# Kernel optimization log

Hardware: AMD Instinct MI355X
Metric: run time of the kernel (lower is better)

The kernel has to match this reference:

```python
import jax, jax.numpy as jnp
import numpy as np

B, S, HID = 2, 2048, 2048
H, KV, D = 16, 4, 128
G = H // KV  # kv groups
THETA = 10000.0


def setup_inputs() -> dict:
    key = jax.random.key(0)
    ks = jax.random.split(key, 6)
    x = jax.random.normal(ks[0], (B, S, HID), dtype=jnp.float32)
    wq = jax.random.normal(ks[1], (HID, H * D), dtype=jnp.float32) * 0.02
    wk = jax.random.normal(ks[2], (HID, KV * D), dtype=jnp.float32) * 0.02
    wv = jax.random.normal(ks[3], (HID, KV * D), dtype=jnp.float32) * 0.02
    wo = jax.random.normal(ks[4], (H * D, HID), dtype=jnp.float32) * 0.02
    # RoPE freqs: complex exp(i * pos * theta^{-2j/D}) -> cos/sin of shape [S, D//2]
    inv_freq = 1.0 / (THETA ** (jnp.arange(0, D, 2, dtype=jnp.float32) / D))
    ang = jnp.arange(S, dtype=jnp.float32)[:, None] * inv_freq[None, :]
    return {"x": x, "freqs_cos": jnp.cos(ang), "freqs_sin": jnp.sin(ang),
            "wq": wq, "wk": wk, "wv": wv, "wo": wo}


def _apply_rope(t, cos, sin):
    # t: [B, h, S, D]; cos/sin: [S, D//2]; complex multiply on interleaved pairs
    tr = t.reshape(*t.shape[:-1], -1, 2)
    x1, x2 = tr[..., 0], tr[..., 1]
    c = cos[None, None, :, :]
    s = sin[None, None, :, :]
    out = jnp.stack([x1 * c - x2 * s, x1 * s + x2 * c], axis=-1)
    return out.reshape(t.shape)


def reference(x, freqs_cos, freqs_sin, wq, wk, wv, wo):
    b, s, _ = x.shape
    q = (x @ wq).reshape(b, s, H, D).transpose(0, 2, 1, 3)   # [B,H,S,D]
    k = (x @ wk).reshape(b, s, KV, D).transpose(0, 2, 1, 3)  # [B,KV,S,D]
    v = (x @ wv).reshape(b, s, KV, D).transpose(0, 2, 1, 3)
    q = _apply_rope(q, freqs_cos, freqs_sin)
    k = _apply_rope(k, freqs_cos, freqs_sin)
    # GQA: group Q heads per KV head instead of expanding K/V
    qg = q.reshape(b, KV, G, s, D)
    scale = 1.0 / jnp.sqrt(jnp.asarray(D, dtype=x.dtype))
    scores = jnp.einsum('bkgqd,bksd->bkgqs', qg, k) * scale  # [B,KV,G,S,S]
    causal = jnp.tril(jnp.ones((s, s), dtype=bool))
    scores = jnp.where(causal[None, None, None], scores, jnp.finfo(scores.dtype).min)
    attn = jax.nn.softmax(scores, axis=-1)
    out = jnp.einsum('bkgqs,bksd->bkgqd', attn, v)           # [B,KV,G,S,D]
    out = out.reshape(b, H, s, D).transpose(0, 2, 1, 3).reshape(b, s, H * D)
    return (out @ wo, k, v)
```

## Files before the change

### kernel.cpp

```cpp
#include <hip/hip_runtime.h>
#include <stdint.h>

#define BB 2
#define SS 2048
#define HIDD 2048
#define HH 16
#define KVH 4
#define DD 128
#define KDIM 2048

typedef short bf16x4 __attribute__((ext_vector_type(4)));
typedef short bf16x8 __attribute__((ext_vector_type(8)));
typedef float f32x4 __attribute__((ext_vector_type(4)));
typedef float f32x16 __attribute__((ext_vector_type(16)));

__device__ __forceinline__ unsigned short f2b(float f) {
  union { float f; unsigned u; } v; v.f = f;
  unsigned r = v.u + 0x7FFFu + ((v.u >> 16) & 1u);
  return (unsigned short)(r >> 16);
}

__device__ __forceinline__ float b2f(unsigned short u) {
  union { unsigned u; float f; } v; v.u = ((unsigned)u) << 16;
  return v.f;
}

__device__ __forceinline__ unsigned cvtpk_bf16(float a, float b) {
  unsigned r;
  asm("v_cvt_pk_bf16_f32 %0, %1, %2" : "=v"(r) : "v"(a), "v"(b));
  return r;
}

__device__ __forceinline__ void gload16(const unsigned short* g, unsigned short* l) {
  __builtin_amdgcn_global_load_lds(
      (const __attribute__((address_space(1))) unsigned int*)(g),
      (__attribute__((address_space(3))) unsigned int*)(l), 16, 0, 0);
}

__device__ __forceinline__ bf16x8 ldT(const char* lds, int byteoff) {
  union { bf16x8 v; int4 q; } u;
  u.q = *reinterpret_cast<const int4*>(lds + byteoff);
  return u.v;
}

template <int N>
__device__ __forceinline__ void waitv() {
  if constexpr (N == 0) asm volatile("s_waitcnt vmcnt(0)" ::: "memory");
  else if constexpr (N == 1) asm volatile("s_waitcnt vmcnt(1)" ::: "memory");
  else if constexpr (N == 2) asm volatile("s_waitcnt vmcnt(2)" ::: "memory");
  else if constexpr (N == 3) asm volatile("s_waitcnt vmcnt(3)" ::: "memory");
  else if constexpr (N == 4) asm volatile("s_waitcnt vmcnt(4)" ::: "memory");
  else if constexpr (N == 5) asm volatile("s_waitcnt vmcnt(5)" ::: "memory");
  else asm volatile("s_waitcnt vmcnt(6)" ::: "memory");
}


__global__ __launch_bounds__(256) void k_convert(const float* __restrict__ in,
                                                 unsigned short* __restrict__ out, int n4) {
  int i = blockIdx.x * 256 + threadIdx.x;
  int stride = gridDim.x * 256;
  for (; i < n4; i += stride) {
    float4 v = reinterpret_cast<const float4*>(in)[i];
    ushort4 o;
    o.x = f2b(v.x); o.y = f2b(v.y); o.z = f2b(v.z); o.w = f2b(v.w);
    int ci = i & 511;
    int t = ci & 7;
    int ci2 = (ci & ~7) | ((t & 3) << 1) | (t >> 2);
    reinterpret_cast<ushort4*>(out)[(i & ~511) | ci2] = o;
  }
}

__global__ __launch_bounds__(256) void k_transpose(const float* __restrict__ in,
                                                   unsigned short* __restrict__ out,
                                                   int K, int N) {
  __shared__ float tile[32][33];
  int n0 = blockIdx.x * 32, k0 = blockIdx.y * 32;
  int tx = threadIdx.x, ty = threadIdx.y;
#pragma unroll
  for (int j = 0; j < 32; j += 8)
    tile[ty + j][tx] = in[(size_t)(k0 + ty + j) * N + n0 + tx];
  __syncthreads();
  int kp = ((tx >> 2) & 3) * 8 + (tx & 3) + ((tx >> 4) << 2);
#pragma unroll
  for (int j = 0; j < 32; j += 8)
    out[(size_t)(n0 + ty + j) * K + k0 + kp] = f2b(tile[tx][ty + j]);
}

__global__ __launch_bounds__(512, 4) void k_gemm12(
    const unsigned short* __restrict__ A, const unsigned short* __restrict__ Bt,
    unsigned short* __restrict__ qws, unsigned short* __restrict__ kws,
    unsigned short* __restrict__ vTws, float* __restrict__ koutF,
    float* __restrict__ voutF, const float* __restrict__ cosT,
    const float* __restrict__ sinT) {
  __shared__ __align__(16) unsigned short lA[2][128 * 64];
  __shared__ __align__(16) unsigned short lB[2][192 * 64];
  const int bid = blockIdx.y * gridDim.x + blockIdx.x;
  const int swz = (bid & 7) * 64 + (bid >> 3);
  const int rowbase = (swz & 31) * 128;
  const int colbase = (swz >> 5) * 192;
  const int tid = threadIdx.x;
  const int wv = tid >> 6, lane = tid & 63;
  const int wr = wv >> 2, wc = wv & 3;
  const int g = lane >> 4, c = lane & 15;

  const unsigned short* aSrc[2];
  const unsigned short* bSrc[3];
  int aDst[2], bDst[3];
#pragma unroll
  for (int j = 0; j < 2; ++j) {
    int idx = j * 512 + tid;
    int row = idx >> 3, sl = idx & 7;
    int gch = sl ^ (row & 7);
    aSrc[j] = A + (size_t)(rowbase + row) * KDIM + gch * 8;
    aDst[j] = idx * 8;
  }
#pragma unroll
  for (int j = 0; j < 3; ++j) {
    int idx = j * 512 + tid;
    int row = idx >> 3, sl = idx & 7;
    int gch = sl ^ (row & 7);
    bSrc[j] = Bt + (size_t)(colbase + row) * KDIM + gch * 8;
    bDst[j] = idx * 8;
  }

  f32x4 acc[4][3] = {};
  const int NT = KDIM / 64;

  auto STAGE = [&](int buf, int kt) {
#pragma unroll
    for (int j = 0; j < 2; ++j)
      gload16(aSrc[j] + kt * 64, &lA[buf][0] + aDst[j]);
#pragma unroll
    for (int j = 0; j < 3; ++j)
      gload16(bSrc[j] + kt * 64, &lB[buf][0] + bDst[j]);
  };

  STAGE(0, 0);
  STAGE(1, 1);

  for (int t = 0; t < NT; ++t) {
    if (t + 1 < NT) { waitv<5>(); } else { waitv<0>(); }
    __builtin_amdgcn_sched_barrier(0);
    __builtin_amdgcn_s_barrier();

    const unsigned short* la = lA[t & 1];
    const unsigned short* lb = lB[t & 1];
    bf16x8 bfr[3][2];
#pragma unroll
    for (int nn = 0; nn < 3; ++nn) {
      int sr = wc * 48 + nn * 16 + c;
#pragma unroll
      for (int kk = 0; kk < 2; ++kk) {
        int slot = (kk * 4 + g) ^ (sr & 7);
        bfr[nn][kk] = *reinterpret_cast<const bf16x8*>(lb + sr * 64 + slot * 8);
      }
    }
#pragma unroll
    for (int mm = 0; mm < 4; ++mm) {
      int sr = wr * 64 + mm * 16 + c;
      int slot0 = g ^ (sr & 7);
      int slot1 = (4 + g) ^ (sr & 7);
      bf16x8 af0 = *reinterpret_cast<const bf16x8*>(la + sr * 64 + slot0 * 8);
      bf16x8 af1 = *reinterpret_cast<const bf16x8*>(la + sr * 64 + slot1 * 8);
#pragma unroll
      for (int nn = 0; nn < 3; ++nn) {
        acc[mm][nn] = __builtin_amdgcn_mfma_f32_16x16x32_bf16(af0, bfr[nn][0], acc[mm][nn], 0, 0, 0);
        acc[mm][nn] = __builtin_amdgcn_mfma_f32_16x16x32_bf16(af1, bfr[nn][1], acc[mm][nn], 0, 0, 0);
      }
    }
    asm volatile("s_waitcnt lgkmcnt(0)" ::: "memory");
    __builtin_amdgcn_s_barrier();
    if (t + 2 < NT) STAGE(t & 1, t + 2);
  }

#pragma unroll
  for (int m = 0; m < 4; ++m) {
#pragma unroll
    for (int n = 0; n < 3; ++n) {
#pragma unroll
      for (int i = 0; i < 4; ++i) {
        float val = acc[m][n][i];
        float partner = __shfl_xor(val, 1, 64);
        int R = rowbase + wr * 64 + m * 16 + g * 4 + i;
        int Cc = colbase + wc * 48 + n * 16 + c;
        int b = R >> 11, s = R & 2047;
        int d = Cc & 127;
        int j = d >> 1;
        float cs = cosT[s * 64 + j], sn = sinT[s * 64 + j];
        float ro = ((d & 1) == 0) ? (val * cs - partner * sn)
                                  : (partner * sn + val * cs);
        if (Cc < 2048) {
          int h = Cc >> 7;
          qws[((size_t)(b * HH + h) * SS + s) * DD + d] = f2b(ro);
        } else if (Cc < 2560) {
          int kvh = (Cc - 2048) >> 7;
          size_t idx = ((size_t)(b * KVH + kvh) * SS + s) * DD + d;
          koutF[idx] = ro;
          int d16 = d & 15;
          int dp = (d & ~15) | (d16 & 3) | ((d16 & 4) << 1) | ((d16 & 8) >> 1);
          kws[((size_t)(b * KVH + kvh) * SS + s) * DD + dp] = f2b(ro);
        } else {
          int kvh = (Cc - 2560) >> 7;
          size_t idx = ((size_t)(b * KVH + kvh) * SS + s) * DD + d;
          voutF[idx] = val;
          int s16 = s & 15;
          int sp = (s & ~15) | (s16 & 3) | ((s16 & 4) << 1) | ((s16 & 8) >> 1);
          vTws[((size_t)(b * KVH + kvh) * DD + d) * SS + sp] = f2b(val);
        }
      }
    }
  }
}

template <int EPI, int BM>
__global__ __launch_bounds__(512) void k_gemm8(
    const unsigned short* __restrict__ A, const unsigned short* __restrict__ Bt,
    float* __restrict__ outF,
    const float* __restrict__ cosT, const float* __restrict__ sinT) {
  constexpr int LA = BM / 128;
  constexpr int LB = 2;
  constexpr int ASTR = BM * 64;
  constexpr int BSTR = 256 * 64;
  constexpr int MF = BM / 64;
  constexpr int LSH = (BM == 256) ? 6 : 5;
  extern __shared__ __align__(16) unsigned short smem[];
  unsigned short* lAb = smem;
  unsigned short* lBb = smem + 2 * ASTR;

  const int bid = blockIdx.y * gridDim.x + blockIdx.x;
  const int nwg = gridDim.x * gridDim.y;
  const int mt = gridDim.x;
  const int swz = (bid & 7) * (nwg >> 3) + (bid >> 3);
  const int rowbase = (swz % mt) * BM;
  const int colbase = (swz / mt) * 256;

  const int tid = threadIdx.x;
  const int wv = tid >> 6, lane = tid & 63;
  const int wr = wv >> 2, wc = wv & 3;
  const int g = lane >> 4, c = lane & 15;

  const int srow8 = lane >> 3;
  const int gch = (lane & 7) ^ srow8;
  const unsigned short* aS[LA][2];
  const unsigned short* bS[2][2];
  int aOff[LA][2], bOff[2][2];
#pragma unroll
  for (int j = 0; j < LA; ++j)
#pragma unroll
    for (int h = 0; h < 2; ++h) {
      int s = wv * LA + j;
      int q = s * 8 + srow8;
      int rA = (q >> LSH) * (BM / 2) + h * (BM / 4) + (q & (BM / 4 - 1));
      aS[j][h] = A + (size_t)(rowbase + rA) * KDIM + gch * 8;
      aOff[j][h] = (h * (BM / 2) + s * 8) * 64;
    }
#pragma unroll
  for (int j = 0; j < 2; ++j)
#pragma unroll
    for (int h = 0; h < 2; ++h) {
      int s = wv * 2 + j;
      int q = s * 8 + srow8;
      int rB = (q >> 5) * 64 + h * 32 + (q & 31);
      bS[j][h] = Bt + (size_t)(colbase + rB) * KDIM + gch * 8;
      bOff[j][h] = (h * 128 + s * 8) * 64;
    }

  f32x4 acc[2 * MF][4] = {};
  bf16x8 af[MF][2], bfr[4][2];
  const int NT = KDIM / 64;

#define STAGE_A(buf, kt, h)                                               \
  _Pragma("unroll") for (int j = 0; j < LA; ++j)                          \
      gload16(aS[j][h] + (kt) * 64, lAb + (buf) * ASTR + aOff[j][h]);
#define STAGE_B(buf, kt, h)                                               \
  _Pragma("unroll") for (int j = 0; j < 2; ++j)                           \
      gload16(bS[j][h] + (kt) * 64, lBb + (buf) * BSTR + bOff[j][h]);
#define LDA(buf, mh)                                                      \
  _Pragma("unroll") for (int mm = 0; mm < MF; ++mm) {                     \
    int sr = (mh) * (BM / 2) + wr * (BM / 4) + mm * 16 + c;               \
    _Pragma("unroll") for (int kk = 0; kk < 2; ++kk) {                    \
      int slot = (kk * 4 + g) ^ (c & 7);                                  \
      af[mm][kk] = *reinterpret_cast<const bf16x8*>(                      \
          lAb + (buf) * ASTR + sr * 64 + slot * 8);                       \
    } }
#define LDB(buf, nh)                                                      \
  _Pragma("unroll") for (int nn = 0; nn < 2; ++nn) {                      \
    int sr = (nh) * 128 + wc * 32 + nn * 16 + c;                          \
    _Pragma("unroll") for (int kk = 0; kk < 2; ++kk) {                    \
      int slot = (kk * 4 + g) ^ (c & 7);                                  \
      bfr[(nh) * 2 + nn][kk] = *reinterpret_cast<const bf16x8*>(          \
          lBb + (buf) * BSTR + sr * 64 + slot * 8);                       \
    } }
#define MM(mh, nh)                                                        \
  _Pragma("unroll") for (int mm = 0; mm < MF; ++mm)                       \
  _Pragma("unroll") for (int nn = 0; nn < 2; ++nn)                        \
  _Pragma("unroll") for (int kk = 0; kk < 2; ++kk)                        \
    acc[(mh) * MF + mm][(nh) * 2 + nn] =                                  \
        __builtin_amdgcn_mfma_f32_16x16x32_bf16(                          \
            af[mm][kk], bfr[(nh) * 2 + nn][kk],                           \
            acc[(mh) * MF + mm][(nh) * 2 + nn], 0, 0, 0);
#define SCHB __builtin_amdgcn_sched_barrier(0);
#define SB __builtin_amdgcn_s_barrier();
#define LGKM asm volatile("s_waitcnt lgkmcnt(0)" ::: "memory");
#define MFMAWIN(mh, nh)                                                   \
  LGKM SCHB __builtin_amdgcn_s_setprio(1);                                \
  MM(mh, nh) __builtin_amdgcn_s_setprio(0); SCHB SB

  STAGE_A(0, 0, 0) STAGE_B(0, 0, 0) STAGE_B(0, 0, 1) STAGE_A(0, 0, 1)
  waitv<LA + LB>(); SCHB SB

  for (int kt = 0; kt < NT - 1; ++kt) {
    const int buf = kt & 1, nbuf = buf ^ 1;
    LDA(buf, 0) LDB(buf, 0)
    STAGE_A(nbuf, kt + 1, 0)
    waitv<2 * LA>(); SCHB SB
    MFMAWIN(0, 0)
    LDB(buf, 1)
    STAGE_B(nbuf, kt + 1, 0)
    waitv<LA + LB>(); SCHB SB
    MFMAWIN(0, 1)
    LDA(buf, 1)
    STAGE_B(nbuf, kt + 1, 1)
    SCHB SB
    MFMAWIN(1, 0)
    STAGE_A(nbuf, kt + 1, 1)
    waitv<LA + LB>(); SCHB SB
    MFMAWIN(1, 1)
  }
  {
    const int buf = (NT - 1) & 1;
    LDA(buf, 0) LDB(buf, 0)
    waitv<LA>(); SCHB SB
    MFMAWIN(0, 0)
    LDB(buf, 1)
    waitv<0>(); SCHB SB
    MFMAWIN(0, 1)
    LDA(buf, 1)
    SCHB SB
    MFMAWIN(1, 0)
    __builtin_amdgcn_s_setprio(1);
    MM(1, 1)
    __builtin_amdgcn_s_setprio(0);
  }

#pragma unroll
  for (int m = 0; m < 2 * MF; ++m)
#pragma unroll
    for (int n = 0; n < 4; ++n)
#pragma unroll
      for (int i = 0; i < 4; ++i) {
        int R = rowbase + wr * (BM / 2) + m * 16 + g * 4 + i;
        int Cc = colbase + wc * 64 + n * 16 + c;
        outF[(size_t)R * 2048 + Cc] = acc[m][n][i];
      }
  (void)cosT; (void)sinT;
#undef STAGE_A
#undef STAGE_B
#undef LDA
#undef LDB
#undef MM
#undef SCHB
#undef SB
#undef LGKM
#undef MFMAWIN
}

__constant__ int JC[24] = {7,15,15,14,14,6,13,13,12,12,5,11,11,10,10,4,9,9,8,8,3,2,1,0};
__constant__ int JP[24] = {0,0,1, 0,1, 0,0,1, 0,1, 0,0,1, 0,1, 0,0,1, 0,1, 0,0,0,0};

__global__ __launch_bounds__(256, 2) void k_attn(const unsigned short* __restrict__ qws,
                                                 const unsigned short* __restrict__ kws,
                                                 const unsigned short* __restrict__ vT,
                                                 unsigned short* __restrict__ aows,
                                                 unsigned short* __restrict__ pO,
                                                 float* __restrict__ pml) {
  __shared__ __align__(16) char lds[2][32768];
  const int tid = threadIdx.x;
  const int lane = tid & 63;
  const int w = tid >> 6;
  const int lq = lane & 31;
  const int hi = lane >> 5;

  const int bid = blockIdx.x;
  const int j = bid >> 5;
  const int y = bid & 31;
  const int head = 4 * (y & 7) + ((y >> 3) & 3);
  const int c = JC[j];
  const int part = JP[j];
  const bool split = (c >= 8);
  const int tstart = split ? (part ? (c + 1) : 0) : 0;
  const int tend = split ? (part ? (2 * c + 2) : (c + 1)) : (2 * c + 2);

  const int b = head >> 4, h = head & 15;
  const int kv = h >> 2;
  const int q0w = c * 128 + w * 32;
  const int qg = q0w + lq;
  const float cl2 = 0.12751743f;

  const unsigned short* qp = qws + ((size_t)(b * HH + h) * SS + qg) * DD;
  bf16x8 qf[8];
#pragma unroll
  for (int ks = 0; ks < 8; ++ks) {
    union { bf16x8 v8; bf16x4 v4[2]; } u;
    const unsigned short* p = qp + ks * 16 + hi * 4;
    u.v4[0] = *reinterpret_cast<const bf16x4*>(p);
    u.v4[1] = *reinterpret_cast<const bf16x4*>(p + 8);
    qf[ks] = u.v8;
  }

  const unsigned short* kbase = kws + (size_t)(b * KVH + kv) * SS * DD;
  const unsigned short* vbase = vT + (size_t)(b * KVH + kv) * DD * SS;

  const unsigned short* kSrc[4];
  const unsigned short* vSrc[4];
  int ldsOff[4];
#pragma unroll
  for (int j2 = 0; j2 < 4; ++j2) {
    int i = w + 4 * j2;
    int ks = i >> 1, half = i & 1;
    kSrc[j2] = kbase + (size_t)(half * 32 + (lane >> 1)) * DD + ks * 16 + (lane & 1) * 8;
    int kkv = i >> 2, d0v = i & 3;
    vSrc[j2] = vbase + (size_t)(d0v * 32 + (lane >> 1)) * SS + kkv * 16 + (lane & 1) * 8;
    ldsOff[j2] = i * 1024;
  }

  auto STAGE = [&](int t, int buf) {
    char* lK = lds[buf];
    char* lV = lds[buf] + 16384;
#pragma unroll
    for (int j2 = 0; j2 < 4; ++j2) {
      gload16(kSrc[j2] + (size_t)t * 64 * DD, (unsigned short*)(lK + ldsOff[j2]));
      gload16(vSrc[j2] + (size_t)t * 64, (unsigned short*)(lV + ldsOff[j2]));
    }
  };

  f32x16 o[4] = {};
  float mrow = -1e30f, lrow = 0.f;

  STAGE(tstart, 0);
  STAGE(tstart + 1, 1);
  asm volatile("s_waitcnt vmcnt(8)" ::: "memory");
  __builtin_amdgcn_sched_barrier(0);
  __builtin_amdgcn_s_barrier();

  for (int t = tstart; t < tend; ++t) {
    const int cur = (t - tstart) & 1;

    if (t * 64 <= q0w + 31) {
      const char* lK = lds[cur];
      const char* lV = lds[cur] + 16384;
      const bool full2 = (t * 64 + 32 <= q0w + 31);

      f32x16 s0 = {}, s1 = {};
      __builtin_amdgcn_s_setprio(1);
#pragma unroll
      for (int ks = 0; ks < 8; ++ks) {
        int off = ks * 2048 + lq * 32 + hi * 16;
        s0 = __builtin_amdgcn_mfma_f32_32x32x16_bf16(ldT(lK, off), qf[ks], s0, 0, 0, 0);
      }
      if (full2) {
#pragma unroll
        for (int ks = 0; ks < 8; ++ks) {
          int off = ks * 2048 + 1024 + lq * 32 + hi * 16;
          s1 = __builtin_amdgcn_mfma_f32_32x32x16_bf16(ldT(lK, off), qf[ks], s1, 0, 0, 0);
        }
      }
      __builtin_amdgcn_s_setprio(0);

      const int kq = t * 64 + 4 * hi - qg;
      float p[32];
      float rowmax = -1e30f;
      const bool m0 = (t * 64 + 31) > q0w;
#pragma unroll
      for (int r = 0; r < 16; ++r) {
        float v = s0[r] * cl2;
        if (m0) {
          int kl = (r & 3) + 8 * (r >> 2);
          if (kq + kl > 0) v = -1e30f;
        }
        p[r] = v;
        rowmax = fmaxf(rowmax, v);
      }
      if (full2) {
        const bool m1 = (t * 64 + 63) > q0w;
#pragma unroll
        for (int r = 0; r < 16; ++r) {
          float v = s1[r] * cl2;
          if (m1) {
            int kl = 32 + (r & 3) + 8 * (r >> 2);
            if (kq + kl > 0) v = -1e30f;
          }
          p[16 + r] = v;
          rowmax = fmaxf(rowmax, v);
        }
      }
      rowmax = fmaxf(rowmax, __shfl_xor(rowmax, 32, 64));

      if (__any(rowmax > mrow + 8.f)) {
        float mnew = fmaxf(mrow, rowmax);
        float fac = exp2f(mrow - mnew);
        mrow = mnew;
        lrow *= fac;
#pragma unroll
        for (int d0 = 0; d0 < 4; ++d0)
#pragma unroll
          for (int r = 0; r < 16; ++r) o[d0][r] *= fac;
      }

      float rsum = 0.f;
#pragma unroll
      for (int e = 0; e < 16; ++e) { p[e] = exp2f(p[e] - mrow); rsum += p[e]; }
      if (full2) {
#pragma unroll
        for (int e = 16; e < 32; ++e) { p[e] = exp2f(p[e] - mrow); rsum += p[e]; }
      }
      rsum += __shfl_xor(rsum, 32, 64);
      lrow += rsum;

      bf16x8 pf[4];
#pragma unroll
      for (int s4 = 0; s4 < 2; ++s4) {
        union { bf16x8 v; unsigned u[4]; } pu;
        int base = s4 * 8;
#pragma unroll
        for (int jj = 0; jj < 4; ++jj)
          pu.u[jj] = cvtpk_bf16(p[base + 2 * jj], p[base + 2 * jj + 1]);
        pf[s4] = pu.v;
      }
      if (full2) {
#pragma unroll
        for (int s4 = 2; s4 < 4; ++s4) {
          union { bf16x8 v; unsigned u[4]; } pu;
          int base = 16 + (s4 - 2) * 8;
#pragma unroll
          for (int jj = 0; jj < 4; ++jj)
            pu.u[jj] = cvtpk_bf16(p[base + 2 * jj], p[base + 2 * jj + 1]);
          pf[s4] = pu.v;
        }
      }

      __builtin_amdgcn_s_setprio(1);
#pragma unroll
      for (int d0 = 0; d0 < 4; ++d0)
#pragma unroll
        for (int kk = 0; kk < 2; ++kk) {
          int off = (kk * 4 + d0) * 1024 + lq * 32 + hi * 16;
          o[d0] = __builtin_amdgcn_mfma_f32_32x32x16_bf16(ldT(lV, off), pf[kk], o[d0], 0, 0, 0);
        }
      if (full2) {
#pragma unroll
        for (int d0 = 0; d0 < 4; ++d0)
#pragma unroll
          for (int kk = 2; kk < 4; ++kk) {
            int off = (kk * 4 + d0) * 1024 + lq * 32 + hi * 16;
            o[d0] = __builtin_amdgcn_mfma_f32_32x32x16_bf16(ldT(lV, off), pf[kk], o[d0], 0, 0, 0);
          }
      }
      __builtin_amdgcn_s_setprio(0);
    }

    if (t + 1 < tend) {
      __builtin_amdgcn_s_barrier();
      if (t + 2 < tend) {
        STAGE(t + 2, cur);
        asm volatile("s_waitcnt vmcnt(8)" ::: "memory");
      } else {
        asm volatile("s_waitcnt vmcnt(0)" ::: "memory");
      }
      __builtin_amdgcn_sched_barrier(0);
      __builtin_amdgcn_s_barrier();
    }
  }

  if (!split) {
    float linv = 1.f / lrow;
    unsigned short* op = aows + ((size_t)(b * SS + qg)) * 2048 + h * 128;
#pragma unroll
    for (int d0 = 0; d0 < 4; ++d0)
#pragma unroll
      for (int rq = 0; rq < 4; ++rq) {
        unsigned w0 = cvtpk_bf16(o[d0][rq * 4 + 0] * linv, o[d0][rq * 4 + 1] * linv);
        unsigned w1 = cvtpk_bf16(o[d0][rq * 4 + 2] * linv, o[d0][rq * 4 + 3] * linv);
        int2 st2; st2.x = (int)w0; st2.y = (int)w1;
        int pos = 8 * ((2 * rq + hi) & 3) + 4 * (rq >> 1);
        *reinterpret_cast<int2*>(op + d0 * 32 + pos) = st2;
      }
  } else {
    int c8 = c - 8;
    int row = qg - c * 128;
    unsigned short* op = pO + ((((size_t)(head * 8 + c8) * 2 + part) * 128) + row) * 128;
#pragma unroll
    for (int d0 = 0; d0 < 4; ++d0)
#pragma unroll
      for (int rq = 0; rq < 4; ++rq) {
        unsigned w0 = cvtpk_bf16(o[d0][rq * 4 + 0], o[d0][rq * 4 + 1]);
        unsigned w1 = cvtpk_bf16(o[d0][rq * 4 + 2], o[d0][rq * 4 + 3]);
        int2 st2; st2.x = (int)w0; st2.y = (int)w1;
        *reinterpret_cast<int2*>(op + d0 * 32 + rq * 8 + hi * 4) = st2;
      }
    if (hi == 0) {
      int mlbase = (((head * 8 + c8) * 2 + part) * 2) * 128 + row;
      pml[mlbase] = mrow;
      pml[mlbase + 128] = lrow;
    }
  }
}

__global__ __launch_bounds__(256) void k_combine(const unsigned short* __restrict__ pO,
                                                 const float* __restrict__ pml,
                                                 unsigned short* __restrict__ aows) {
  int tid = blockIdx.x * 256 + threadIdx.x;
  int rg = tid >> 4;
  int d8 = tid & 15;
  int head = rg >> 10;
  int rem = rg & 1023;
  int c8 = rem >> 7;
  int row = rem & 127;
  int base2 = (head * 8 + c8) * 2;

  float m1 = pml[((base2 + 0) * 2 + 0) * 128 + row];
  float l1 = pml[((base2 + 0) * 2 + 1) * 128 + row];
  float m2 = pml[((base2 + 1) * 2 + 0) * 128 + row];
  float l2 = pml[((base2 + 1) * 2 + 1) * 128 + row];
  float m = fmaxf(m1, m2);
  float w1 = exp2f(m1 - m), w2 = exp2f(m2 - m);
  float inv = 1.f / (w1 * l1 + w2 * l2);

  const unsigned short* o1 = pO + (((size_t)(base2 + 0) * 128 + row) * 128) + d8 * 8;
  const unsigned short* o2 = pO + (((size_t)(base2 + 1) * 128 + row) * 128) + d8 * 8;
  union { int4 q; unsigned short us[8]; } ua, ub;
  ua.q = *reinterpret_cast<const int4*>(o1);
  ub.q = *reinterpret_cast<const int4*>(o2);
  float out[8];
#pragma unroll
  for (int e = 0; e < 8; ++e)
    out[e] = (w1 * b2f(ua.us[e]) + w2 * b2f(ub.us[e])) * inv;

  int b = head >> 4, h = head & 15;
  int s = (c8 + 8) * 128 + row;
  unsigned short* dst = aows + ((size_t)(b * SS + s)) * 2048 + h * 128;
  int d = d8 * 8;
  int dbase = d & ~31;
#pragma unroll
  for (int jj = 0; jj < 2; ++jj) {
    int t = ((d >> 2) + jj) & 7;
    int pos = ((t & 3) << 3) + ((t >> 2) << 2);
    unsigned wa = cvtpk_bf16(out[jj * 4 + 0], out[jj * 4 + 1]);
    unsigned wb = cvtpk_bf16(out[jj * 4 + 2], out[jj * 4 + 3]);
    int2 st2; st2.x = (int)wa; st2.y = (int)wb;
    *reinterpret_cast<int2*>(dst + dbase + pos) = st2;
  }
}

extern "C" void kernel_launch(void* const* d_in, const int* in_sizes, int n_in,
                              void* d_out, int out_size, void* d_ws, size_t ws_size,
                              hipStream_t stream) {
  (void)in_sizes; (void)n_in; (void)out_size; (void)ws_size;
  const float* x  = (const float*)d_in[0];
  const float* fc = (const float*)d_in[1];
  const float* fs = (const float*)d_in[2];
  const float* wq = (const float*)d_in[3];
  const float* wk = (const float*)d_in[4];
  const float* wv = (const float*)d_in[5];
  const float* wo = (const float*)d_in[6];
  float* out = (float*)d_out;
  float* koutF = out + (size_t)BB * SS * HIDD;
  float* voutF = koutF + (size_t)BB * KVH * SS * DD;

  unsigned short* wcatT = (unsigned short*)d_ws;
  unsigned short* woT   = wcatT + (size_t)3072 * 2048;
  unsigned short* xbf   = woT + (size_t)2048 * 2048;
  unsigned short* qws   = xbf + (size_t)4096 * 2048;
  unsigned short* kws   = qws + (size_t)BB * HH * SS * DD;
  unsigned short* vTws  = kws + (size_t)BB * KVH * SS * DD;
  unsigned short* aows  = vTws + (size_t)BB * KVH * DD * SS;

  unsigned short* pO = xbf;
  float* pml = (float*)wcatT;

  hipFuncSetAttribute((const void*)k_gemm8<0, 128>,
                      hipFuncAttributeMaxDynamicSharedMemorySize, 98304);

  k_convert<<<2048, 256, 0, stream>>>(x, xbf, (int)((size_t)4096 * 2048 / 4));
  dim3 tb(32, 8);
  k_transpose<<<dim3(64, 64), tb, 0, stream>>>(wq, wcatT, 2048, 2048);
  k_transpose<<<dim3(16, 64), tb, 0, stream>>>(wk, wcatT + (size_t)2048 * 2048, 2048, 512);
  k_transpose<<<dim3(16, 64), tb, 0, stream>>>(wv, wcatT + (size_t)2560 * 2048, 2048, 512);
  k_transpose<<<dim3(64, 64), tb, 0, stream>>>(wo, woT, 2048, 2048);

  k_gemm12<<<dim3(32, 16), 512, 0, stream>>>(xbf, wcatT, qws, kws, vTws,
                                             koutF, voutF, fc, fs);
  k_attn<<<768, 256, 0, stream>>>(qws, kws, vTws, aows, pO, pml);
  k_combine<<<2048, 256, 0, stream>>>(pO, pml, aows);
  k_gemm8<0, 128><<<dim3(32, 8), 512, 98304, stream>>>(aows, woT, out, nullptr, nullptr);
}
```

Measured before the change: 216.8 us.

## Double attention block to 256 query rows with 8 waves sharing K/V tiles

The attention kernel now uses 512 threads per block, with each block covering 256 query rows instead of 128. Eight waves share each staged K/V tile, so the global-to-LDS traffic per query row is halved. The causal work schedule and split-KV tables are rebuilt for the coarser chunks, and the partial-output layout and the combine kernel are remapped to match. The cost is half as many blocks (384), which can hurt load balance across CUs, plus larger per-block synchronisation barriers.

```diff
diff --git a/kernel.cpp b/kernel.cpp
--- a/kernel.cpp
+++ b/kernel.cpp
@@ -365,10 +365,10 @@
 #undef MFMAWIN
 }
 
-__constant__ int JC[24] = {7,15,15,14,14,6,13,13,12,12,5,11,11,10,10,4,9,9,8,8,3,2,1,0};
-__constant__ int JP[24] = {0,0,1, 0,1, 0,0,1, 0,1, 0,0,1, 0,1, 0,0,1, 0,1, 0,0,0,0};
-
-__global__ __launch_bounds__(256, 2) void k_attn(const unsigned short* __restrict__ qws,
+__constant__ int JC[12] = {3,7,7,6,6,5,5,2,4,4,1,0};
+__constant__ int JP[12] = {0,0,1,0,1,0,1,0,0,1,0,0};
+
+__global__ __launch_bounds__(512, 4) void k_attn(const unsigned short* __restrict__ qws,
                                                  const unsigned short* __restrict__ kws,
                                                  const unsigned short* __restrict__ vT,
                                                  unsigned short* __restrict__ aows,
@@ -387,13 +387,13 @@
   const int head = 4 * (y & 7) + ((y >> 3) & 3);
   const int c = JC[j];
   const int part = JP[j];
-  const bool split = (c >= 8);
-  const int tstart = split ? (part ? (c + 1) : 0) : 0;
-  const int tend = split ? (part ? (2 * c + 2) : (c + 1)) : (2 * c + 2);
+  const bool split = (c >= 4);
+  const int tstart = (split && part) ? 2 * (c + 1) : 0;
+  const int tend = split ? (part ? 4 * (c + 1) : 2 * (c + 1)) : 4 * (c + 1);
 
   const int b = head >> 4, h = head & 15;
   const int kv = h >> 2;
-  const int q0w = c * 128 + w * 32;
+  const int q0w = c * 256 + w * 32;
   const int qg = q0w + lq;
   const float cl2 = 0.12751743f;
 
@@ -411,12 +411,12 @@
   const unsigned short* kbase = kws + (size_t)(b * KVH + kv) * SS * DD;
   const unsigned short* vbase = vT + (size_t)(b * KVH + kv) * DD * SS;
 
-  const unsigned short* kSrc[4];
-  const unsigned short* vSrc[4];
-  int ldsOff[4];
-#pragma unroll
-  for (int j2 = 0; j2 < 4; ++j2) {
-    int i = w + 4 * j2;
+  const unsigned short* kSrc[2];
+  const unsigned short* vSrc[2];
+  int ldsOff[2];
+#pragma unroll
+  for (int j2 = 0; j2 < 2; ++j2) {
+    int i = w + 8 * j2;
     int ks = i >> 1, half = i & 1;
     kSrc[j2] = kbase + (size_t)(half * 32 + (lane >> 1)) * DD + ks * 16 + (lane & 1) * 8;
     int kkv = i >> 2, d0v = i & 3;
@@ -428,7 +428,7 @@
     char* lK = lds[buf];
     char* lV = lds[buf] + 16384;
 #pragma unroll
-    for (int j2 = 0; j2 < 4; ++j2) {
+    for (int j2 = 0; j2 < 2; ++j2) {
       gload16(kSrc[j2] + (size_t)t * 64 * DD, (unsigned short*)(lK + ldsOff[j2]));
       gload16(vSrc[j2] + (size_t)t * 64, (unsigned short*)(lV + ldsOff[j2]));
     }
@@ -439,7 +439,7 @@
 
   STAGE(tstart, 0);
   STAGE(tstart + 1, 1);
-  asm volatile("s_waitcnt vmcnt(8)" ::: "memory");
+  waitv<4>();
   __builtin_amdgcn_sched_barrier(0);
   __builtin_amdgcn_s_barrier();
 
@@ -563,9 +563,9 @@
       __builtin_amdgcn_s_barrier();
       if (t + 2 < tend) {
         STAGE(t + 2, cur);
-        asm volatile("s_waitcnt vmcnt(8)" ::: "memory");
+        waitv<4>();
       } else {
-        asm volatile("s_waitcnt vmcnt(0)" ::: "memory");
+        waitv<0>();
       }
       __builtin_amdgcn_sched_barrier(0);
       __builtin_amdgcn_s_barrier();
@@ -586,9 +586,9 @@
         *reinterpret_cast<int2*>(op + d0 * 32 + pos) = st2;
       }
   } else {
-    int c8 = c - 8;
-    int row = qg - c * 128;
-    unsigned short* op = pO + ((((size_t)(head * 8 + c8) * 2 + part) * 128) + row) * 128;
+    int slot = (head * 4 + (c - 4)) * 2 + part;
+    int row = qg - c * 256;
+    unsigned short* op = pO + ((size_t)slot * 256 + row) * 128;
 #pragma unroll
     for (int d0 = 0; d0 < 4; ++d0)
 #pragma unroll
@@ -599,9 +599,8 @@
         *reinterpret_cast<int2*>(op + d0 * 32 + rq * 8 + hi * 4) = st2;
       }
     if (hi == 0) {
-      int mlbase = (((head * 8 + c8) * 2 + part) * 2) * 128 + row;
-      pml[mlbase] = mrow;
-      pml[mlbase + 128] = lrow;
+      pml[slot * 512 + row] = mrow;
+      pml[slot * 512 + 256 + row] = lrow;
     }
   }
 }
@@ -610,24 +609,24 @@
                                                  const float* __restrict__ pml,
                                                  unsigned short* __restrict__ aows) {
   int tid = blockIdx.x * 256 + threadIdx.x;
+  int d8 = tid & 15;
   int rg = tid >> 4;
-  int d8 = tid & 15;
-  int head = rg >> 10;
-  int rem = rg & 1023;
-  int c8 = rem >> 7;
-  int row = rem & 127;
-  int base2 = (head * 8 + c8) * 2;
-
-  float m1 = pml[((base2 + 0) * 2 + 0) * 128 + row];
-  float l1 = pml[((base2 + 0) * 2 + 1) * 128 + row];
-  float m2 = pml[((base2 + 1) * 2 + 0) * 128 + row];
-  float l2 = pml[((base2 + 1) * 2 + 1) * 128 + row];
+  int row = rg & 255;
+  int rem = rg >> 8;
+  int c4 = rem & 3;
+  int head = rem >> 2;
+  int s1 = (head * 4 + c4) * 2, s2 = s1 + 1;
+
+  float m1 = pml[s1 * 512 + row];
+  float l1 = pml[s1 * 512 + 256 + row];
+  float m2 = pml[s2 * 512 + row];
+  float l2 = pml[s2 * 512 + 256 + row];
   float m = fmaxf(m1, m2);
   float w1 = exp2f(m1 - m), w2 = exp2f(m2 - m);
   float inv = 1.f / (w1 * l1 + w2 * l2);
 
-  const unsigned short* o1 = pO + (((size_t)(base2 + 0) * 128 + row) * 128) + d8 * 8;
-  const unsigned short* o2 = pO + (((size_t)(base2 + 1) * 128 + row) * 128) + d8 * 8;
+  const unsigned short* o1 = pO + ((size_t)s1 * 256 + row) * 128 + d8 * 8;
+  const unsigned short* o2 = pO + ((size_t)s2 * 256 + row) * 128 + d8 * 8;
   union { int4 q; unsigned short us[8]; } ua, ub;
   ua.q = *reinterpret_cast<const int4*>(o1);
   ub.q = *reinterpret_cast<const int4*>(o2);
@@ -637,7 +636,7 @@
     out[e] = (w1 * b2f(ua.us[e]) + w2 * b2f(ub.us[e])) * inv;
 
   int b = head >> 4, h = head & 15;
-  int s = (c8 + 8) * 128 + row;
+  int s = (c4 + 4) * 256 + row;
   unsigned short* dst = aows + ((size_t)(b * SS + s)) * 2048 + h * 128;
   int d = d8 * 8;
   int dbase = d & ~31;
@@ -690,7 +689,7 @@
 
   k_gemm12<<<dim3(32, 16), 512, 0, stream>>>(xbf, wcatT, qws, kws, vTws,
                                              koutF, voutF, fc, fs);
-  k_attn<<<768, 256, 0, stream>>>(qws, kws, vTws, aows, pO, pml);
+  k_attn<<<384, 512, 0, stream>>>(qws, kws, vTws, aows, pO, pml);
   k_combine<<<2048, 256, 0, stream>>>(pO, pml, aows);
   k_gemm8<0, 128><<<dim3(32, 8), 512, 98304, stream>>>(aows, woT, out, nullptr, nullptr);
 }
```

Measured after the change: 681.3 us. +214.3%, slower.
